# Optimization experiments

Measured on AMD Instinct MI355X. Metric: run time of the kernel, lower is better.

Reference implementation:

```python
import jax, jax.numpy as jnp
import numpy as np

DIM = 1024
HEADS = 16
DIM_HEAD = 64
INNER = HEADS * DIM_HEAD  # 1024
SCALE = DIM_HEAD ** -0.5


def setup_inputs() -> dict:
    key = jax.random.key(0)
    k1, k2, k3, k4 = jax.random.split(key, 4)
    B, N = 4, 2048
    x = jax.random.normal(k1, (B, N, DIM), dtype=jnp.float32)
    # Linear weights stored as [in, out] so y = x @ W (+ b)
    W_qkv = jax.random.normal(k2, (DIM, 3 * INNER), dtype=jnp.float32) * (DIM ** -0.5)
    W_out = jax.random.normal(k3, (INNER, DIM), dtype=jnp.float32) * (INNER ** -0.5)
    b_out = jax.random.normal(k4, (DIM,), dtype=jnp.float32) * 0.01
    return {"x": x, "W_qkv": W_qkv, "W_out": W_out, "b_out": b_out}


def reference(x, W_qkv, W_out, b_out):
    B, N, _ = x.shape
    qkv = x @ W_qkv  # [B, N, 3*INNER]
    q, k, v = jnp.split(qkv, 3, axis=-1)
    # [B, N, H, Dh] -> [B, H, N, Dh]
    reshape = lambda t: t.reshape(B, N, HEADS, DIM_HEAD).transpose(0, 2, 1, 3)
    q, k, v = reshape(q), reshape(k), reshape(v)
    dots = jnp.einsum("bhqd,bhkd->bhqk", q, k) * SCALE  # [B,H,N,N]
    attn = jax.nn.softmax(dots, axis=-1)
    out = jnp.einsum("bhqk,bhkd->bhqd", attn, v)  # [B,H,N,Dh]
    out = out.transpose(0, 2, 1, 3).reshape(B, N, INNER)
    return out @ W_out + b_out
```

## Files before the change

### kernel.cpp

```cpp
#include <hip/hip_runtime.h>


typedef _Float16 half8 __attribute__((ext_vector_type(8)));
typedef __fp16 fp16v2 __attribute__((ext_vector_type(2)));
typedef float floatx4 __attribute__((ext_vector_type(4)));
typedef unsigned short u16;

struct __align__(8) U16x4 { u16 x, y, z, w; };

__device__ __forceinline__ u16 f2h(float f) {
  union { _Float16 h; u16 u; } cv;
  cv.h = (_Float16)f;
  return cv.u;
}

__device__ __forceinline__ void g2l16(const void* g, void* l) {
  __builtin_amdgcn_global_load_lds(
      (const __attribute__((address_space(1))) void*)g,
      (__attribute__((address_space(3))) void*)l, 16, 0, 0);
}

__device__ __forceinline__ int swz(int c) { return (c & 3) ^ ((c >> 3) & 3); }
__device__ __forceinline__ int swz8(int s) { return (s & 7) ^ ((s >> 3) & 7); }

__global__ __launch_bounds__(256) void cast_f32_f16(const float* __restrict__ in,
                                                    u16* __restrict__ out) {
  long long base = ((long long)blockIdx.x * 256 + threadIdx.x) * 8;
  float4 a = *(const float4*)(in + base);
  float4 b = *(const float4*)(in + base + 4);
  U16x4 u0 = {f2h(a.x), f2h(a.y), f2h(a.z), f2h(a.w)};
  U16x4 u1 = {f2h(b.x), f2h(b.y), f2h(b.z), f2h(b.w)};
  *(U16x4*)(out + base) = u0;
  *(U16x4*)(out + base + 4) = u1;
}

__global__ __launch_bounds__(256) void transpose_cast(const float* __restrict__ in,
                                                      u16* __restrict__ out,
                                                      int K, int N) {
  __shared__ u16 ls[64][72];
  const int nTK = K >> 6;
  const int tk = blockIdx.x % nTK;
  const int tn = blockIdx.x / nTK;
  const int tid = threadIdx.x;
#pragma unroll
  for (int i = 0; i < 4; ++i) {
    int idx = i * 256 + tid;
    int r = idx >> 4, c4 = (idx & 15) * 4;
    float4 v = *(const float4*)(in + (long long)(tk * 64 + r) * N + tn * 64 + c4);
    ls[r][c4 + 0] = f2h(v.x);
    ls[r][c4 + 1] = f2h(v.y);
    ls[r][c4 + 2] = f2h(v.z);
    ls[r][c4 + 3] = f2h(v.w);
  }
  __syncthreads();
#pragma unroll
  for (int i = 0; i < 4; ++i) {
    int idx = i * 256 + tid;
    int nr = idx >> 4, kc4 = (idx & 15) * 4;
    U16x4 u = {ls[kc4 + 0][nr], ls[kc4 + 1][nr], ls[kc4 + 2][nr], ls[kc4 + 3][nr]};
    *(U16x4*)(out + (long long)(tn * 64 + nr) * K + tk * 64 + kc4) = u;
  }
}

template <int EPI>
__global__ __launch_bounds__(256, 4) void gemm_f16(const u16* __restrict__ A,
                                                   const u16* __restrict__ Bt,
                                                   u16* __restrict__ O0,
                                                   u16* __restrict__ O1,
                                                   u16* __restrict__ O2,
                                                   float* __restrict__ Of,
                                                   const float* __restrict__ bias) {
  __shared__ __attribute__((aligned(16))) u16 lsA[128 * 64];
  __shared__ __attribute__((aligned(16))) u16 lsB[128 * 64];
  const int tid = threadIdx.x;
  const int lane = tid & 63, wave = tid >> 6;
  const int l15 = lane & 15, quad = lane >> 4;
  const int w7 = l15 & 7;
  const int offk0 = ((quad) ^ w7) * 8;
  const int offk1 = ((4 + quad) ^ w7) * 8;
  const int wm = (wave >> 1) * 64, wn = (wave & 1) * 64;
  const int bm = blockIdx.x & 63;
  const int bn = blockIdx.x >> 6;

  const u16* ga[4];
  const u16* gb[4];
#pragma unroll
  for (int i = 0; i < 4; ++i) {
    int s = i * 256 + tid;
    ga[i] = A + (long long)(bm * 128 + (s >> 3)) * 1024 + swz8(s) * 8;
    gb[i] = Bt + (long long)(bn * 128 + (s >> 3)) * 1024 + swz8(s) * 8;
  }

  floatx4 acc[4][4] = {};

  for (int kt = 0; kt < 16; ++kt) {
    const int ko = kt * 64;
#pragma unroll
    for (int i = 0; i < 4; ++i)
      g2l16(ga[i] + ko, lsA + (i * 256 + wave * 64) * 8);
#pragma unroll
    for (int i = 0; i < 4; ++i)
      g2l16(gb[i] + ko, lsB + (i * 256 + wave * 64) * 8);
    __syncthreads();
#pragma unroll
    for (int ks = 0; ks < 2; ++ks) {
      const int off = ks ? offk1 : offk0;
      half8 af[4], bf[4];
#pragma unroll
      for (int mt = 0; mt < 4; ++mt)
        af[mt] = *(const half8*)(lsA + (wm + mt * 16 + l15) * 64 + off);
#pragma unroll
      for (int nt = 0; nt < 4; ++nt)
        bf[nt] = *(const half8*)(lsB + (wn + nt * 16 + l15) * 64 + off);
#pragma unroll
      for (int mt = 0; mt < 4; ++mt)
#pragma unroll
        for (int nt = 0; nt < 4; ++nt)
          acc[mt][nt] = __builtin_amdgcn_mfma_f32_16x16x32_f16(af[mt], bf[nt], acc[mt][nt], 0, 0, 0);
    }
    __syncthreads();
  }

  if (EPI == 0) {
    const float slq = 0.125f * 1.44269504088896f;
#pragma unroll
    for (int mt = 0; mt < 4; ++mt) {
      int gm = bm * 128 + wm + mt * 16 + quad * 4;
      int b = gm >> 11, n0 = gm & 2047;
#pragma unroll
      for (int nt = 0; nt < 4; ++nt) {
        int gc = bn * 128 + wn + nt * 16 + l15;
        int t = gc >> 10, hd = gc & 1023, h = hd >> 6, d = hd & 63;
        long long bh = (long long)(b * 16 + h);
        if (t == 2) {
          U16x4 u = {f2h(acc[mt][nt][0]), f2h(acc[mt][nt][1]),
                     f2h(acc[mt][nt][2]), f2h(acc[mt][nt][3])};
          *(U16x4*)(O2 + (bh * 64 + d) * 2048 + n0) = u;
        } else {
          float s = (t == 0) ? slq : 1.0f;
          u16* dst = (t == 0 ? O0 : O1) + (bh * 2048 + n0) * 64 + d;
#pragma unroll
          for (int r = 0; r < 4; ++r) dst[r * 64] = f2h(acc[mt][nt][r] * s);
        }
      }
    }
  } else {
#pragma unroll
    for (int mt = 0; mt < 4; ++mt) {
      int gm = bm * 128 + wm + mt * 16 + quad * 4;
#pragma unroll
      for (int nt = 0; nt < 4; ++nt) {
        int gc = bn * 128 + wn + nt * 16 + l15;
        float bv = bias[gc];
#pragma unroll
        for (int r = 0; r < 4; ++r)
          Of[(long long)(gm + r) * 1024 + gc] = acc[mt][nt][r] + bv;
      }
    }
  }
}

__global__ __launch_bounds__(256, 2) void attn_flash(const u16* __restrict__ Qh,
                                                     const u16* __restrict__ Kh,
                                                     const u16* __restrict__ Vt,
                                                     u16* __restrict__ Oh) {
  __shared__ __attribute__((aligned(16))) u16 lsK[2 * 2 * 64 * 32];
  __shared__ __attribute__((aligned(16))) u16 lsV[2 * 2 * 64 * 32];
  __shared__ __attribute__((aligned(16))) u16 lsP[4 * 64 * 32];
  const int tid = threadIdx.x;
  const int lane = tid & 63, wave = tid >> 6;
  const int l15 = lane & 15, quad = lane >> 4;
  const int sw = (l15 >> 1) & 3;
  const int qsw8 = (quad ^ sw) * 8;
  const int bh = blockIdx.x & 63, qt = blockIdx.x >> 6;
  const u16* Qb = Qh + ((long long)bh * 2048 + qt * 256) * 64;
  const u16* Kb = Kh + (long long)bh * 2048 * 64;
  const u16* Vb = Vt + (long long)bh * 64 * 2048;
  u16* lsPw = lsP + wave * 2048;

  half8 qb[4][2];
#pragma unroll
  for (int pass = 0; pass < 2; ++pass) {
#pragma unroll
    for (int i = 0; i < 4; ++i) {
      int c = i * 256 + tid;
      g2l16(Qb + (pass * 128 + ((c >> 2) & 127)) * 64 + (c >> 9) * 32 + swz(c) * 8,
            lsK + (i * 256 + wave * 64) * 8);
    }
    __syncthreads();
    if ((wave >> 1) == pass) {
      const int lrow = (wave & 1) * 64;
#pragma unroll
      for (int qt2 = 0; qt2 < 4; ++qt2)
#pragma unroll
        for (int ks = 0; ks < 2; ++ks)
          qb[qt2][ks] = *(const half8*)(lsK + ks * 4096 +
                                        (lrow + qt2 * 16 + l15) * 32 + qsw8);
    }
    __syncthreads();
  }

#pragma unroll
  for (int i = 0; i < 2; ++i) {
    int c = i * 256 + tid;
    g2l16(Kb + ((c >> 2) & 63) * 64 + (c >> 8) * 32 + swz(c) * 8,
          lsK + (i * 256 + wave * 64) * 8);
    g2l16(Vb + ((c >> 2) & 63) * 2048 + (c >> 8) * 32 + swz(c) * 8,
          lsV + (i * 256 + wave * 64) * 8);
  }

  half8 onesf;
#pragma unroll
  for (int j = 0; j < 8; ++j) onesf[j] = (_Float16)1.0f;

  floatx4 oacc[4][4] = {};
  floatx4 osum[4] = {};

  for (int kt = 0; kt < 32; ++kt) {
    const int cur = kt & 1;
    const u16* bufK = lsK + cur * 4096;
    const u16* bufV = lsV + cur * 4096;
    __syncthreads();
    if (kt < 31) {
      u16* nK = lsK + (1 - cur) * 4096;
      u16* nV = lsV + (1 - cur) * 4096;
#pragma unroll
      for (int i = 0; i < 2; ++i) {
        int c = i * 256 + tid;
        g2l16(Kb + (kt + 1) * 4096 + ((c >> 2) & 63) * 64 + (c >> 8) * 32 + swz(c) * 8,
              nK + (i * 256 + wave * 64) * 8);
        g2l16(Vb + ((c >> 2) & 63) * 2048 + (kt + 1) * 64 + (c >> 8) * 32 + swz(c) * 8,
              nV + (i * 256 + wave * 64) * 8);
      }
    }
#pragma unroll
    for (int ks4 = 0; ks4 < 2; ++ks4) {
      floatx4 sacc[2][4] = {};
#pragma unroll
      for (int ks = 0; ks < 2; ++ks) {
#pragma unroll
        for (int h = 0; h < 2; ++h) {
          half8 kf = *(const half8*)(bufK + ks * 2048 + ((ks4 * 2 + h) * 16 + l15) * 32 + qsw8);
#pragma unroll
          for (int qt2 = 0; qt2 < 4; ++qt2)
            sacc[h][qt2] = __builtin_amdgcn_mfma_f32_16x16x32_f16(kf, qb[qt2][ks], sacc[h][qt2], 0, 0, 0);
        }
      }
#pragma unroll
      for (int h = 0; h < 2; ++h) {
#pragma unroll
        for (int qt2 = 0; qt2 < 4; ++qt2) {
          float p0 = __builtin_amdgcn_exp2f(sacc[h][qt2][0]);
          float p1 = __builtin_amdgcn_exp2f(sacc[h][qt2][1]);
          float p2 = __builtin_amdgcn_exp2f(sacc[h][qt2][2]);
          float p3 = __builtin_amdgcn_exp2f(sacc[h][qt2][3]);
          union { fp16v2 h2; unsigned u; } lo, hi;
          lo.h2 = __builtin_amdgcn_cvt_pkrtz(p0, p1);
          hi.h2 = __builtin_amdgcn_cvt_pkrtz(p2, p3);
          uint2 pk = {lo.u, hi.u};
          *(uint2*)(lsPw + (qt2 * 16 + l15) * 32 +
                    (((2 * h + (quad >> 1)) ^ sw) * 8) + (quad & 1) * 4) = pk;
        }
      }
      half8 pa[4];
#pragma unroll
      for (int qt2 = 0; qt2 < 4; ++qt2)
        pa[qt2] = *(const half8*)(lsPw + (qt2 * 16 + l15) * 32 + qsw8);
#pragma unroll
      for (int dt = 0; dt < 4; ++dt) {
        half8 vb = *(const half8*)(bufV + ks4 * 2048 + (dt * 16 + l15) * 32 + qsw8);
#pragma unroll
        for (int qt2 = 0; qt2 < 4; ++qt2)
          oacc[qt2][dt] = __builtin_amdgcn_mfma_f32_16x16x32_f16(pa[qt2], vb, oacc[qt2][dt], 0, 0, 0);
      }
#pragma unroll
      for (int qt2 = 0; qt2 < 4; ++qt2)
        osum[qt2] = __builtin_amdgcn_mfma_f32_16x16x32_f16(pa[qt2], onesf, osum[qt2], 0, 0, 0);
    }
  }

  const int b = bh >> 4, h = bh & 15;
#pragma unroll
  for (int qt2 = 0; qt2 < 4; ++qt2) {
#pragma unroll
    for (int r = 0; r < 4; ++r) {
      float inv = 1.0f / osum[qt2][r];
      int qrow = qt * 256 + wave * 64 + qt2 * 16 + quad * 4 + r;
      long long rowbase = ((long long)b * 2048 + qrow) * 1024 + h * 64;
#pragma unroll
      for (int dt = 0; dt < 4; ++dt)
        Oh[rowbase + dt * 16 + l15] = f2h(oacc[qt2][dt][r] * inv);
    }
  }
}

extern "C" void kernel_launch(void* const* d_in, const int* in_sizes, int n_in,
                              void* d_out, int out_size, void* d_ws, size_t ws_size,
                              hipStream_t stream) {
  const float* x = (const float*)d_in[0];
  const float* Wqkv = (const float*)d_in[1];
  const float* Wout = (const float*)d_in[2];
  const float* bout = (const float*)d_in[3];
  float* out = (float*)d_out;

  char* ws = (char*)d_ws;
  u16* Xh = (u16*)(ws);
  u16* Wqkvt = (u16*)(ws + (16ll << 20));
  u16* Woutt = (u16*)(ws + (22ll << 20));
  u16* Qh = (u16*)(ws + (24ll << 20));
  u16* Kh = (u16*)(ws + (40ll << 20));
  u16* Vt = (u16*)(ws + (56ll << 20));
  u16* Oh = (u16*)(ws + (72ll << 20));

  cast_f32_f16<<<4096, 256, 0, stream>>>(x, Xh);
  transpose_cast<<<16 * 48, 256, 0, stream>>>(Wqkv, Wqkvt, 1024, 3072);
  transpose_cast<<<16 * 16, 256, 0, stream>>>(Wout, Woutt, 1024, 1024);
  gemm_f16<0><<<64 * 24, 256, 0, stream>>>(Xh, Wqkvt, Qh, Kh, Vt, nullptr, nullptr);
  attn_flash<<<512, 256, 0, stream>>>(Qh, Kh, Vt, Oh);
  gemm_f16<1><<<64 * 8, 256, 0, stream>>>(Oh, Woutt, nullptr, nullptr, nullptr, out, bout);
}
```

Before: 244.5 us.

## Triple-buffer GEMM K-loop, fuse prep kernels, add MFMA priority hints in attention

The GEMM now streams K in 32-wide slices through a three-stage LDS ring, prefetching two slices ahead with explicit vmcnt waits and raw barriers, so global loads overlap MFMA work instead of being serialized with it. The occupancy hint drops from 4 to 3 blocks per CU to fit the larger LDS footprint. The three cast/transpose prep kernels are merged into one launch to cut launch overhead. The attention kernel raises wave priority around its MFMA blocks to favour matrix issue. The risks are lower occupancy and fragile hand-written waitcnt handling.

```diff
diff --git a/kernel.cpp b/kernel.cpp
--- a/kernel.cpp
+++ b/kernel.cpp
@@ -21,27 +21,33 @@
 }
 
 __device__ __forceinline__ int swz(int c) { return (c & 3) ^ ((c >> 3) & 3); }
-__device__ __forceinline__ int swz8(int s) { return (s & 7) ^ ((s >> 3) & 7); }
-
-__global__ __launch_bounds__(256) void cast_f32_f16(const float* __restrict__ in,
-                                                    u16* __restrict__ out) {
-  long long base = ((long long)blockIdx.x * 256 + threadIdx.x) * 8;
-  float4 a = *(const float4*)(in + base);
-  float4 b = *(const float4*)(in + base + 4);
-  U16x4 u0 = {f2h(a.x), f2h(a.y), f2h(a.z), f2h(a.w)};
-  U16x4 u1 = {f2h(b.x), f2h(b.y), f2h(b.z), f2h(b.w)};
-  *(U16x4*)(out + base) = u0;
-  *(U16x4*)(out + base + 4) = u1;
-}
-
-__global__ __launch_bounds__(256) void transpose_cast(const float* __restrict__ in,
-                                                      u16* __restrict__ out,
-                                                      int K, int N) {
+
+__global__ __launch_bounds__(256) void prep(const float* __restrict__ x,
+                                            u16* __restrict__ Xh,
+                                            const float* __restrict__ Wqkv,
+                                            u16* __restrict__ Wqkvt,
+                                            const float* __restrict__ Wout,
+                                            u16* __restrict__ Woutt) {
   __shared__ u16 ls[64][72];
-  const int nTK = K >> 6;
-  const int tk = blockIdx.x % nTK;
-  const int tn = blockIdx.x / nTK;
+  const int bid = blockIdx.x;
   const int tid = threadIdx.x;
+  if (bid < 4096) {
+    long long base = ((long long)bid * 256 + tid) * 8;
+    float4 a = *(const float4*)(x + base);
+    float4 b = *(const float4*)(x + base + 4);
+    U16x4 u0 = {f2h(a.x), f2h(a.y), f2h(a.z), f2h(a.w)};
+    U16x4 u1 = {f2h(b.x), f2h(b.y), f2h(b.z), f2h(b.w)};
+    *(U16x4*)(Xh + base) = u0;
+    *(U16x4*)(Xh + base + 4) = u1;
+    return;
+  }
+  const float* in;
+  u16* out;
+  int N, tile;
+  if (bid < 4096 + 768) { in = Wqkv; out = Wqkvt; N = 3072; tile = bid - 4096; }
+  else                  { in = Wout; out = Woutt; N = 1024; tile = bid - 4864; }
+  const int K = 1024, nTK = 16;
+  const int tk = tile % nTK, tn = tile / nTK;
 #pragma unroll
   for (int i = 0; i < 4; ++i) {
     int idx = i * 256 + tid;
@@ -63,62 +69,78 @@
 }
 
 template <int EPI>
-__global__ __launch_bounds__(256, 4) void gemm_f16(const u16* __restrict__ A,
+__global__ __launch_bounds__(256, 3) void gemm_f16(const u16* __restrict__ A,
                                                    const u16* __restrict__ Bt,
                                                    u16* __restrict__ O0,
                                                    u16* __restrict__ O1,
                                                    u16* __restrict__ O2,
                                                    float* __restrict__ Of,
                                                    const float* __restrict__ bias) {
-  __shared__ __attribute__((aligned(16))) u16 lsA[128 * 64];
-  __shared__ __attribute__((aligned(16))) u16 lsB[128 * 64];
+  __shared__ __attribute__((aligned(16))) u16 lsA[3 * 4096];
+  __shared__ __attribute__((aligned(16))) u16 lsB[3 * 4096];
   const int tid = threadIdx.x;
   const int lane = tid & 63, wave = tid >> 6;
   const int l15 = lane & 15, quad = lane >> 4;
-  const int w7 = l15 & 7;
-  const int offk0 = ((quad) ^ w7) * 8;
-  const int offk1 = ((4 + quad) ^ w7) * 8;
+  const int rdoff = (quad ^ ((l15 >> 1) & 3)) * 8;
   const int wm = (wave >> 1) * 64, wn = (wave & 1) * 64;
-  const int bm = blockIdx.x & 63;
-  const int bn = blockIdx.x >> 6;
-
-  const u16* ga[4];
-  const u16* gb[4];
-#pragma unroll
-  for (int i = 0; i < 4; ++i) {
-    int s = i * 256 + tid;
-    ga[i] = A + (long long)(bm * 128 + (s >> 3)) * 1024 + swz8(s) * 8;
-    gb[i] = Bt + (long long)(bn * 128 + (s >> 3)) * 1024 + swz8(s) * 8;
+  const int bm = blockIdx.x & 63, bn = blockIdx.x >> 6;
+
+  const u16* gA[2];
+  const u16* gB[2];
+  int dst[2];
+#pragma unroll
+  for (int j = 0; j < 2; ++j) {
+    int sl = j * 256 + tid;
+    int r = sl >> 2, cc = sl & 3;
+    int csw = (cc ^ ((r >> 1) & 3)) * 8;
+    gA[j] = A + (long long)(bm * 128 + r) * 1024 + csw;
+    gB[j] = Bt + (long long)(bn * 128 + r) * 1024 + csw;
+    dst[j] = sl * 8;
   }
 
   floatx4 acc[4][4] = {};
 
-  for (int kt = 0; kt < 16; ++kt) {
-    const int ko = kt * 64;
+#pragma unroll
+  for (int t = 0; t < 2; ++t) {
+#pragma unroll
+    for (int j = 0; j < 2; ++j) g2l16(gA[j] + t * 32, lsA + t * 4096 + dst[j]);
+#pragma unroll
+    for (int j = 0; j < 2; ++j) g2l16(gB[j] + t * 32, lsB + t * 4096 + dst[j]);
+  }
+  asm volatile("s_waitcnt vmcnt(4)");
+  __builtin_amdgcn_s_barrier();
+
+  int cur = 0;
+  for (int t = 0; t < 32; ++t) {
+    const u16* bA = lsA + cur * 4096;
+    const u16* bB = lsB + cur * 4096;
+    half8 af[4], bf[4];
 #pragma unroll
     for (int i = 0; i < 4; ++i)
-      g2l16(ga[i] + ko, lsA + (i * 256 + wave * 64) * 8);
+      af[i] = *(const half8*)(bA + (wm + i * 16 + l15) * 32 + rdoff);
 #pragma unroll
     for (int i = 0; i < 4; ++i)
-      g2l16(gb[i] + ko, lsB + (i * 256 + wave * 64) * 8);
-    __syncthreads();
-#pragma unroll
-    for (int ks = 0; ks < 2; ++ks) {
-      const int off = ks ? offk1 : offk0;
-      half8 af[4], bf[4];
-#pragma unroll
-      for (int mt = 0; mt < 4; ++mt)
-        af[mt] = *(const half8*)(lsA + (wm + mt * 16 + l15) * 64 + off);
+      bf[i] = *(const half8*)(bB + (wn + i * 16 + l15) * 32 + rdoff);
+    if (t < 30) {
+      const int nb = cur ? cur - 1 : 2;
+      const int ko = (t + 2) * 32;
+#pragma unroll
+      for (int j = 0; j < 2; ++j) g2l16(gA[j] + ko, lsA + nb * 4096 + dst[j]);
+#pragma unroll
+      for (int j = 0; j < 2; ++j) g2l16(gB[j] + ko, lsB + nb * 4096 + dst[j]);
+    }
+    __builtin_amdgcn_s_barrier();
+    asm volatile("s_waitcnt lgkmcnt(0)");
+#pragma unroll
+    for (int mt = 0; mt < 4; ++mt)
 #pragma unroll
       for (int nt = 0; nt < 4; ++nt)
-        bf[nt] = *(const half8*)(lsB + (wn + nt * 16 + l15) * 64 + off);
-#pragma unroll
-      for (int mt = 0; mt < 4; ++mt)
-#pragma unroll
-        for (int nt = 0; nt < 4; ++nt)
-          acc[mt][nt] = __builtin_amdgcn_mfma_f32_16x16x32_f16(af[mt], bf[nt], acc[mt][nt], 0, 0, 0);
-    }
-    __syncthreads();
+        acc[mt][nt] = __builtin_amdgcn_mfma_f32_16x16x32_f16(af[mt], bf[nt],
+                                                             acc[mt][nt], 0, 0, 0);
+    if (t < 30)       asm volatile("s_waitcnt vmcnt(4)");
+    else if (t == 30) asm volatile("s_waitcnt vmcnt(0)");
+    __builtin_amdgcn_s_barrier();
+    cur = cur == 2 ? 0 : cur + 1;
   }
 
   if (EPI == 0) {
@@ -130,17 +152,17 @@
 #pragma unroll
       for (int nt = 0; nt < 4; ++nt) {
         int gc = bn * 128 + wn + nt * 16 + l15;
-        int t = gc >> 10, hd = gc & 1023, h = hd >> 6, d = hd & 63;
+        int tsel = gc >> 10, hd = gc & 1023, h = hd >> 6, d = hd & 63;
         long long bh = (long long)(b * 16 + h);
-        if (t == 2) {
+        if (tsel == 2) {
           U16x4 u = {f2h(acc[mt][nt][0]), f2h(acc[mt][nt][1]),
                      f2h(acc[mt][nt][2]), f2h(acc[mt][nt][3])};
           *(U16x4*)(O2 + (bh * 64 + d) * 2048 + n0) = u;
         } else {
-          float s = (t == 0) ? slq : 1.0f;
-          u16* dst = (t == 0 ? O0 : O1) + (bh * 2048 + n0) * 64 + d;
-#pragma unroll
-          for (int r = 0; r < 4; ++r) dst[r * 64] = f2h(acc[mt][nt][r] * s);
+          float s = (tsel == 0) ? slq : 1.0f;
+          u16* dstp = (tsel == 0 ? O0 : O1) + (bh * 2048 + n0) * 64 + d;
+#pragma unroll
+          for (int r = 0; r < 4; ++r) dstp[r * 64] = f2h(acc[mt][nt][r] * s);
         }
       }
     }
@@ -236,6 +258,7 @@
 #pragma unroll
     for (int ks4 = 0; ks4 < 2; ++ks4) {
       floatx4 sacc[2][4] = {};
+      __builtin_amdgcn_s_setprio(1);
 #pragma unroll
       for (int ks = 0; ks < 2; ++ks) {
 #pragma unroll
@@ -246,6 +269,7 @@
             sacc[h][qt2] = __builtin_amdgcn_mfma_f32_16x16x32_f16(kf, qb[qt2][ks], sacc[h][qt2], 0, 0, 0);
         }
       }
+      __builtin_amdgcn_s_setprio(0);
 #pragma unroll
       for (int h = 0; h < 2; ++h) {
 #pragma unroll
@@ -266,6 +290,7 @@
 #pragma unroll
       for (int qt2 = 0; qt2 < 4; ++qt2)
         pa[qt2] = *(const half8*)(lsPw + (qt2 * 16 + l15) * 32 + qsw8);
+      __builtin_amdgcn_s_setprio(1);
 #pragma unroll
       for (int dt = 0; dt < 4; ++dt) {
         half8 vb = *(const half8*)(bufV + ks4 * 2048 + (dt * 16 + l15) * 32 + qsw8);
@@ -276,6 +301,7 @@
 #pragma unroll
       for (int qt2 = 0; qt2 < 4; ++qt2)
         osum[qt2] = __builtin_amdgcn_mfma_f32_16x16x32_f16(pa[qt2], onesf, osum[qt2], 0, 0, 0);
+      __builtin_amdgcn_s_setprio(0);
     }
   }
 
@@ -312,10 +338,8 @@
   u16* Vt = (u16*)(ws + (56ll << 20));
   u16* Oh = (u16*)(ws + (72ll << 20));
 
-  cast_f32_f16<<<4096, 256, 0, stream>>>(x, Xh);
-  transpose_cast<<<16 * 48, 256, 0, stream>>>(Wqkv, Wqkvt, 1024, 3072);
-  transpose_cast<<<16 * 16, 256, 0, stream>>>(Wout, Woutt, 1024, 1024);
-  gemm_f16<0><<<64 * 24, 256, 0, stream>>>(Xh, Wqkvt, Qh, Kh, Vt, nullptr, nullptr);
+  prep<<<5120, 256, 0, stream>>>(x, Xh, Wqkv, Wqkvt, Wout, Woutt);
+  gemm_f16<0><<<1536, 256, 0, stream>>>(Xh, Wqkvt, Qh, Kh, Vt, nullptr, nullptr);
   attn_flash<<<512, 256, 0, stream>>>(Qh, Kh, Vt, Oh);
-  gemm_f16<1><<<64 * 8, 256, 0, stream>>>(Oh, Woutt, nullptr, nullptr, nullptr, out, bout);
-}
+  gemm_f16<1><<<512, 256, 0, stream>>>(Oh, Woutt, nullptr, nullptr, nullptr, out, bout);
+}
```

Result: no change. 245.7 us (+0.5%).

## Merge prep kernels into one launch and raise wave priority around attention MFMAs

Applied to the files above, without the earlier changes.

Folds the x cast and the two weight transpose-casts into a single prep kernel, dispatched by block index, which cuts two kernel launches and the gaps between them. Separately, the attention inner loop raises wave priority with s_setprio around the QK and PV MFMA blocks, so the scheduler favours waves issuing matrix ops while others do exp and LDS work. The prep kernel now carries the transpose's shared memory even for cast blocks, which may lower occupancy for those blocks.

```diff
diff --git a/kernel.cpp b/kernel.cpp
--- a/kernel.cpp
+++ b/kernel.cpp
@@ -23,25 +23,32 @@
 __device__ __forceinline__ int swz(int c) { return (c & 3) ^ ((c >> 3) & 3); }
 __device__ __forceinline__ int swz8(int s) { return (s & 7) ^ ((s >> 3) & 7); }
 
-__global__ __launch_bounds__(256) void cast_f32_f16(const float* __restrict__ in,
-                                                    u16* __restrict__ out) {
-  long long base = ((long long)blockIdx.x * 256 + threadIdx.x) * 8;
-  float4 a = *(const float4*)(in + base);
-  float4 b = *(const float4*)(in + base + 4);
-  U16x4 u0 = {f2h(a.x), f2h(a.y), f2h(a.z), f2h(a.w)};
-  U16x4 u1 = {f2h(b.x), f2h(b.y), f2h(b.z), f2h(b.w)};
-  *(U16x4*)(out + base) = u0;
-  *(U16x4*)(out + base + 4) = u1;
-}
-
-__global__ __launch_bounds__(256) void transpose_cast(const float* __restrict__ in,
-                                                      u16* __restrict__ out,
-                                                      int K, int N) {
+__global__ __launch_bounds__(256) void prep(const float* __restrict__ x,
+                                            u16* __restrict__ Xh,
+                                            const float* __restrict__ Wqkv,
+                                            u16* __restrict__ Wqkvt,
+                                            const float* __restrict__ Wout,
+                                            u16* __restrict__ Woutt) {
   __shared__ u16 ls[64][72];
-  const int nTK = K >> 6;
-  const int tk = blockIdx.x % nTK;
-  const int tn = blockIdx.x / nTK;
+  const int bid = blockIdx.x;
   const int tid = threadIdx.x;
+  if (bid < 4096) {
+    long long base = ((long long)bid * 256 + tid) * 8;
+    float4 a = *(const float4*)(x + base);
+    float4 b = *(const float4*)(x + base + 4);
+    U16x4 u0 = {f2h(a.x), f2h(a.y), f2h(a.z), f2h(a.w)};
+    U16x4 u1 = {f2h(b.x), f2h(b.y), f2h(b.z), f2h(b.w)};
+    *(U16x4*)(Xh + base) = u0;
+    *(U16x4*)(Xh + base + 4) = u1;
+    return;
+  }
+  const float* in;
+  u16* out;
+  int N, tile;
+  if (bid < 4096 + 768) { in = Wqkv; out = Wqkvt; N = 3072; tile = bid - 4096; }
+  else                  { in = Wout; out = Woutt; N = 1024; tile = bid - 4864; }
+  const int K = 1024, nTK = 16;
+  const int tk = tile % nTK, tn = tile / nTK;
 #pragma unroll
   for (int i = 0; i < 4; ++i) {
     int idx = i * 256 + tid;
@@ -236,6 +243,7 @@
 #pragma unroll
     for (int ks4 = 0; ks4 < 2; ++ks4) {
       floatx4 sacc[2][4] = {};
+      __builtin_amdgcn_s_setprio(1);
 #pragma unroll
       for (int ks = 0; ks < 2; ++ks) {
 #pragma unroll
@@ -246,6 +254,7 @@
             sacc[h][qt2] = __builtin_amdgcn_mfma_f32_16x16x32_f16(kf, qb[qt2][ks], sacc[h][qt2], 0, 0, 0);
         }
       }
+      __builtin_amdgcn_s_setprio(0);
 #pragma unroll
       for (int h = 0; h < 2; ++h) {
 #pragma unroll
@@ -266,6 +275,7 @@
 #pragma unroll
       for (int qt2 = 0; qt2 < 4; ++qt2)
         pa[qt2] = *(const half8*)(lsPw + (qt2 * 16 + l15) * 32 + qsw8);
+      __builtin_amdgcn_s_setprio(1);
 #pragma unroll
       for (int dt = 0; dt < 4; ++dt) {
         half8 vb = *(const half8*)(bufV + ks4 * 2048 + (dt * 16 + l15) * 32 + qsw8);
@@ -276,6 +286,7 @@
 #pragma unroll
       for (int qt2 = 0; qt2 < 4; ++qt2)
         osum[qt2] = __builtin_amdgcn_mfma_f32_16x16x32_f16(pa[qt2], onesf, osum[qt2], 0, 0, 0);
+      __builtin_amdgcn_s_setprio(0);
     }
   }
 
@@ -312,9 +323,7 @@
   u16* Vt = (u16*)(ws + (56ll << 20));
   u16* Oh = (u16*)(ws + (72ll << 20));
 
-  cast_f32_f16<<<4096, 256, 0, stream>>>(x, Xh);
-  transpose_cast<<<16 * 48, 256, 0, stream>>>(Wqkv, Wqkvt, 1024, 3072);
-  transpose_cast<<<16 * 16, 256, 0, stream>>>(Wout, Woutt, 1024, 1024);
+  prep<<<5120, 256, 0, stream>>>(x, Xh, Wqkv, Wqkvt, Wout, Woutt);
   gemm_f16<0><<<64 * 24, 256, 0, stream>>>(Xh, Wqkvt, Qh, Kh, Vt, nullptr, nullptr);
   attn_flash<<<512, 256, 0, stream>>>(Qh, Kh, Vt, Oh);
   gemm_f16<1><<<64 * 8, 256, 0, stream>>>(Oh, Woutt, nullptr, nullptr, nullptr, out, bout);
```

Result: slower. 252.2 us (+3.2%).
